# Performance work log

Measured on AMD Instinct MI355X. Metric: run time of the kernel, lower is better.

Reference implementation:

```python
import jax, jax.numpy as jnp
import numpy as np

HIDDEN_DIM = 1024
NUM_HEADS = 8
CONTEXT_LEN = 8
HEAD_DIM = HIDDEN_DIM // NUM_HEADS


def setup_inputs() -> dict:
    key = jax.random.key(0)
    ks = jax.random.split(key, 6)
    B, C, H, W = 32, HIDDEN_DIM, 18, 32
    K = CONTEXT_LEN
    h_current = jax.random.normal(ks[0], (B, C, H, W), dtype=jnp.float32)
    h_buffer = jax.random.normal(ks[1], (K, B, C, H, W), dtype=jnp.float32)
    # Parameters (torch nn.Linear stores weight as [out, in]; y = x @ W.T + b)
    s_qkv = 1.0 / np.sqrt(C)
    W_qkv = jax.random.uniform(ks[2], (3 * C, C), jnp.float32, -s_qkv, s_qkv)
    W_out = jax.random.uniform(ks[3], (C, C), jnp.float32, -s_qkv, s_qkv)
    b_out = jax.random.uniform(ks[4], (C,), jnp.float32, -s_qkv, s_qkv)
    rel_emb = jax.random.normal(ks[5], (2 * CONTEXT_LEN + 1, NUM_HEADS), dtype=jnp.float32)
    return {"h_current": h_current, "h_buffer": h_buffer, "W_qkv": W_qkv,
            "W_out": W_out, "b_out": b_out, "rel_emb": rel_emb}


def reference(h_current, h_buffer, W_qkv, W_out, b_out, rel_emb):
    B, C, H, W = h_current.shape
    K = h_buffer.shape[0]
    T = K + 1
    nh, hd = NUM_HEADS, HEAD_DIM

    # spatial pooling (AdaptiveAvgPool2d(1)) then stack buffer frames + current
    pooled_buf = h_buffer.mean(axis=(3, 4))          # [K, B, C]
    pooled_cur = h_current.mean(axis=(2, 3))         # [B, C]
    context = jnp.concatenate(
        [jnp.transpose(pooled_buf, (1, 0, 2)), pooled_cur[:, None, :]], axis=1)  # [B, T, C]

    # QKV projection (no bias)
    qkv = context @ W_qkv.T                          # [B, T, 3C]
    q, k, v = jnp.split(qkv, 3, axis=-1)
    q = q.reshape(B, T, nh, hd).transpose(0, 2, 1, 3)  # [B, nh, T, hd]
    k = k.reshape(B, T, nh, hd).transpose(0, 2, 1, 3)
    v = v.reshape(B, T, nh, hd).transpose(0, 2, 1, 3)

    # relative-position bias
    idx = jnp.arange(T)
    rel = jnp.clip(idx[:, None] - idx[None, :], -CONTEXT_LEN, CONTEXT_LEN) + CONTEXT_LEN
    bias = rel_emb[rel]                              # [T, T, nh]
    bias = jnp.transpose(bias, (2, 0, 1))            # [nh, T, T]

    # causal mask (-inf above diagonal) combined with bias
    causal = jnp.triu(jnp.full((T, T), -jnp.inf, dtype=context.dtype), k=1)
    attn_mask = causal[None, None, :, :] + bias[None, :, :, :]  # [1, nh, T, T]

    scale = 1.0 / np.sqrt(hd)
    scores = jnp.einsum('bhqd,bhkd->bhqk', q, k) * scale + attn_mask
    attn = jax.nn.softmax(scores, axis=-1)
    attn_out = jnp.einsum('bhqk,bhkd->bhqd', attn, v)  # [B, nh, T, hd]
    attn_out = attn_out.transpose(0, 2, 1, 3).reshape(B, T, C)

    # output projection of final timestep, broadcast over spatial dims, residual
    out = attn_out[:, -1] @ W_out.T + b_out          # [B, C]
    return h_current + out[:, :, None, None]
```

## Files before the change

kernel.cpp:

```cpp
#include <hip/hip_runtime.h>
#include <hip/hip_bf16.h>

#define BB 32
#define CC 1024
#define HWSZ 576
#define KCTX 8
#define TT 9
#define NH 8
#define HD 128

#define GBM 32
#define GBN 128
#define GBK 32

#define NS_KV 8
#define NS_Q  8

#define KV_MN (288 * 2048)
#define Q_MN  (32 * 1024)

typedef float v4f __attribute__((ext_vector_type(4)));

__global__ __launch_bounds__(256) void pool_kernel(
    const float* __restrict__ hbuf,
    const float* __restrict__ hcur,
    float* __restrict__ ctx)
{
    const int wave = threadIdx.x >> 6;
    const int lane = threadIdx.x & 63;
    const int sub  = lane >> 4;
    const int l16  = lane & 15;
    const int stride = gridDim.x * 16;
    const int nrows = BB * TT * CC;

    for (int r0 = (blockIdx.x * 4 + wave) * 4; r0 < nrows; r0 += stride) {
        const int r = r0 + sub;
        v4f acc = {0.f, 0.f, 0.f, 0.f};
        int cidx;
        if (r < KCTX * BB * CC) {
            const v4f* s4 = (const v4f*)(hbuf + (size_t)r * HWSZ);
            const int t = r >> 15;
            const int b = (r >> 10) & 31;
            cidx = (b * TT + t) * CC + (r & (CC - 1));
#pragma unroll
            for (int j = 0; j < 9; ++j)
                acc += __builtin_nontemporal_load(s4 + l16 + 16 * j);
        } else {
            const int rc = r - KCTX * BB * CC;
            const v4f* s4 = (const v4f*)(hcur + (size_t)rc * HWSZ);
            cidx = ((rc >> 10) * TT + KCTX) * CC + (rc & (CC - 1));
#pragma unroll
            for (int j = 0; j < 9; ++j)
                acc += s4[l16 + 16 * j];
        }
        float sum = acc.x + acc.y + acc.z + acc.w;
        sum += __shfl_xor(sum, 1);
        sum += __shfl_xor(sum, 2);
        sum += __shfl_xor(sum, 4);
        sum += __shfl_xor(sum, 8);
        if (l16 == 0) ctx[cidx] = sum * (1.0f / 576.0f);
    }
}

__device__ __forceinline__ void gemm_tile_body(
    const float* __restrict__ Ablk, int lda,
    const float* __restrict__ Bblk, int ldb,
    float* __restrict__ Yout, int ldy,
    int k0, int klen,
    float (*As)[GBK + 4], float (*Bs)[GBN + 4])
{
    const int tid = threadIdx.x;
    const int tx = tid & 15;
    const int ty = tid >> 4;

    float acc0[8], acc1[8];
#pragma unroll
    for (int i = 0; i < 8; ++i) { acc0[i] = 0.f; acc1[i] = 0.f; }

    for (int kt = k0; kt < k0 + klen; kt += GBK) {
        {
            const int row = tid >> 3;
            const int kc = (tid & 7) << 2;
            float4 a = *(const float4*)(Ablk + (size_t)row * lda + kt + kc);
            *(float4*)(&As[row][kc]) = a;
        }
        {
            const int kc = (tid & 7) << 2;
            const int r0 = tid >> 3;
#pragma unroll
            for (int rr = 0; rr < 4; ++rr) {
                const int row = r0 + rr * 32;
                float4 bv = *(const float4*)(Bblk + (size_t)row * ldb + kt + kc);
                Bs[kc + 0][row] = bv.x;
                Bs[kc + 1][row] = bv.y;
                Bs[kc + 2][row] = bv.z;
                Bs[kc + 3][row] = bv.w;
            }
        }
        __syncthreads();

#pragma unroll
        for (int k4 = 0; k4 < GBK; k4 += 4) {
            float4 a0 = *(const float4*)(&As[ty * 2 + 0][k4]);
            float4 a1 = *(const float4*)(&As[ty * 2 + 1][k4]);
            const float a0v[4] = {a0.x, a0.y, a0.z, a0.w};
            const float a1v[4] = {a1.x, a1.y, a1.z, a1.w};
#pragma unroll
            for (int i = 0; i < 4; ++i) {
                float4 blo = *(const float4*)(&Bs[k4 + i][tx * 8]);
                float4 bhi = *(const float4*)(&Bs[k4 + i][tx * 8 + 4]);
                acc0[0] += a0v[i] * blo.x;  acc0[1] += a0v[i] * blo.y;
                acc0[2] += a0v[i] * blo.z;  acc0[3] += a0v[i] * blo.w;
                acc0[4] += a0v[i] * bhi.x;  acc0[5] += a0v[i] * bhi.y;
                acc0[6] += a0v[i] * bhi.z;  acc0[7] += a0v[i] * bhi.w;
                acc1[0] += a1v[i] * blo.x;  acc1[1] += a1v[i] * blo.y;
                acc1[2] += a1v[i] * blo.z;  acc1[3] += a1v[i] * blo.w;
                acc1[4] += a1v[i] * bhi.x;  acc1[5] += a1v[i] * bhi.y;
                acc1[6] += a1v[i] * bhi.z;  acc1[7] += a1v[i] * bhi.w;
            }
        }
        __syncthreads();
    }

    const int col = tx * 8;
    const int row0 = ty * 2;
    float* y0 = Yout + (size_t)row0 * ldy + col;
    float* y1 = y0 + ldy;
    *(float4*)(y0 + 0) = make_float4(acc0[0], acc0[1], acc0[2], acc0[3]);
    *(float4*)(y0 + 4) = make_float4(acc0[4], acc0[5], acc0[6], acc0[7]);
    *(float4*)(y1 + 0) = make_float4(acc1[0], acc1[1], acc1[2], acc1[3]);
    *(float4*)(y1 + 4) = make_float4(acc1[4], acc1[5], acc1[6], acc1[7]);
}

__global__ __launch_bounds__(256) void qkv_gemm(
    const float* __restrict__ ctx, const float* __restrict__ Wqkv,
    float* __restrict__ qpart, float* __restrict__ kvpart)
{
    __shared__ float As[GBM][GBK + 4];
    __shared__ float Bs[GBK][GBN + 4];

    const int bid = blockIdx.x;
    if (bid < NS_Q * 8) {
        const int s = bid & (NS_Q - 1);
        const int bn = bid >> 3;
        gemm_tile_body(ctx + 8 * CC, TT * CC,
                       Wqkv + (size_t)bn * GBN * CC, CC,
                       qpart + (size_t)s * Q_MN + bn * GBN, 1024,
                       s * (1024 / NS_Q), 1024 / NS_Q, As, Bs);
    } else {
        const int rel = bid - NS_Q * 8;
        const int s = rel & (NS_KV - 1);
        const int tile = rel >> 3;
        const int bm = tile >> 4;
        const int bn = tile & 15;
        gemm_tile_body(ctx + (size_t)bm * GBM * CC, CC,
                       Wqkv + (size_t)CC * CC + (size_t)bn * GBN * CC, CC,
                       kvpart + (size_t)s * KV_MN + (size_t)bm * GBM * 2048 + bn * GBN, 2048,
                       s * (1024 / NS_KV), 1024 / NS_KV, As, Bs);
    }
}

__global__ __launch_bounds__(64) void attn_kernel(
    const float* __restrict__ kvpart,
    const float* __restrict__ qpart,
    const float* __restrict__ rel_emb,
    float* __restrict__ attn_out)
{
    const int lane = threadIdx.x;
    const int pair = blockIdx.x;
    const int b = pair >> 3;
    const int h = pair & 7;
    const float scale = 0.08838834764831845f;

    const int qoff = b * CC + h * HD;
    float q1 = 0.f, q2 = 0.f;
#pragma unroll
    for (int s = 0; s < NS_Q; ++s) {
        q1 += qpart[(size_t)s * Q_MN + qoff + lane];
        q2 += qpart[(size_t)s * Q_MN + qoff + lane + 64];
    }
    q1 *= scale; q2 *= scale;

    float sc[TT];
#pragma unroll
    for (int j = 0; j < TT; ++j) {
        const size_t base = (size_t)(b * TT + j) * 2048 + h * HD;
        float k1 = 0.f, k2 = 0.f;
#pragma unroll
        for (int s = 0; s < NS_KV; ++s) {
            k1 += kvpart[(size_t)s * KV_MN + base + lane];
            k2 += kvpart[(size_t)s * KV_MN + base + lane + 64];
        }
        float p = q1 * k1 + q2 * k2;
#pragma unroll
        for (int off = 32; off; off >>= 1) p += __shfl_xor(p, off);
        sc[j] = p + rel_emb[(2 * KCTX - j) * NH + h];
    }
    float m = sc[0];
#pragma unroll
    for (int j = 1; j < TT; ++j) m = fmaxf(m, sc[j]);
    float sum = 0.f;
#pragma unroll
    for (int j = 0; j < TT; ++j) { sc[j] = expf(sc[j] - m); sum += sc[j]; }
    const float inv = 1.0f / sum;

    float a1 = 0.f, a2 = 0.f;
#pragma unroll
    for (int j = 0; j < TT; ++j) {
        const size_t base = (size_t)(b * TT + j) * 2048 + 1024 + h * HD;
        float v1 = 0.f, v2 = 0.f;
#pragma unroll
        for (int s = 0; s < NS_KV; ++s) {
            v1 += kvpart[(size_t)s * KV_MN + base + lane];
            v2 += kvpart[(size_t)s * KV_MN + base + lane + 64];
        }
        a1 += sc[j] * v1;
        a2 += sc[j] * v2;
    }
    attn_out[qoff + lane] = a1 * inv;
    attn_out[qoff + lane + 64] = a2 * inv;
}

__global__ __launch_bounds__(256) void final_fused(
    const float* __restrict__ hc,
    const float* __restrict__ attnb,
    const float* __restrict__ Wout,
    const float* __restrict__ bias,
    float* __restrict__ y)
{
    const int wave = threadIdx.x >> 6;
    const int lane = threadIdx.x & 63;
    const int stride = gridDim.x * 4;
    const int nrows = BB * CC;

    for (int r = blockIdx.x * 4 + wave; r < nrows; r += stride) {
        const int b = r >> 10;
        const int c = r & (CC - 1);

        const v4f* ar = (const v4f*)(attnb + (size_t)b * CC);
        const v4f* wr = (const v4f*)(Wout + (size_t)c * CC);
        v4f acc = {0.f, 0.f, 0.f, 0.f};
#pragma unroll
        for (int j = 0; j < 4; ++j) {
            v4f a = ar[lane + 64 * j];
            v4f w = wr[lane + 64 * j];
            acc += a * w;
        }
        float dot = acc.x + acc.y + acc.z + acc.w;
#pragma unroll
        for (int off = 32; off; off >>= 1) dot += __shfl_xor(dot, off);
        const float add = dot + bias[c];

        const v4f* s4 = (const v4f*)(hc + (size_t)r * HWSZ);
        v4f* d4 = (v4f*)(y + (size_t)r * HWSZ);
        v4f v0 = s4[lane];
        v0.x += add; v0.y += add; v0.z += add; v0.w += add;
        __builtin_nontemporal_store(v0, d4 + lane);
        v4f v1 = s4[lane + 64];
        v1.x += add; v1.y += add; v1.z += add; v1.w += add;
        __builtin_nontemporal_store(v1, d4 + lane + 64);
        if (lane < 16) {
            v4f v2 = s4[lane + 128];
            v2.x += add; v2.y += add; v2.z += add; v2.w += add;
            __builtin_nontemporal_store(v2, d4 + lane + 128);
        }
    }
}

extern "C" void kernel_launch(void* const* d_in, const int* in_sizes, int n_in,
                              void* d_out, int out_size, void* d_ws, size_t ws_size,
                              hipStream_t stream) {
    const float* h_current = (const float*)d_in[0];
    const float* h_buffer  = (const float*)d_in[1];
    const float* W_qkv     = (const float*)d_in[2];
    const float* W_out     = (const float*)d_in[3];
    const float* b_out     = (const float*)d_in[4];
    const float* rel_emb   = (const float*)d_in[5];

    float* ws = (float*)d_ws;
    float* ctx    = ws;
    float* kvpart = ctx + 294912;
    float* qpart  = kvpart + (size_t)NS_KV * KV_MN;
    float* attnb  = qpart + (size_t)NS_Q * Q_MN;

    pool_kernel<<<2048, 256, 0, stream>>>(h_buffer, h_current, ctx);

    qkv_gemm<<<NS_Q * 8 + NS_KV * 144, 256, 0, stream>>>(ctx, W_qkv, qpart, kvpart);

    attn_kernel<<<BB * NH, 64, 0, stream>>>(kvpart, qpart, rel_emb, attnb);

    final_fused<<<2048, 256, 0, stream>>>(h_current, attnb, W_out, b_out, (float*)d_out);
}
```

Before: 165.1 us.

## Replace FP32 QKV GEMM with bf16 MFMA and convert weights in pool kernel

The QKV projection now runs on bf16 MFMA 16x16x32 instructions. Each wave computes a 16x128 tile directly from global memory, with split-K reduced from 8 to 4, which also shrinks the partial buffers the attention kernel has to sum. The pool kernel writes the pooled context as bf16 and converts W_qkv to bf16 on every call. This trades the scalar-FMA GEMM for matrix cores at the cost of an extra weight conversion pass each call and reduced precision.

```diff
diff --git a/kernel.cpp b/kernel.cpp
--- a/kernel.cpp
+++ b/kernel.cpp
@@ -9,22 +9,26 @@
 #define NH 8
 #define HD 128
 
-#define GBM 32
-#define GBN 128
-#define GBK 32
-
-#define NS_KV 8
-#define NS_Q  8
-
+#define NS 4
 #define KV_MN (288 * 2048)
 #define Q_MN  (32 * 1024)
 
 typedef float v4f __attribute__((ext_vector_type(4)));
+typedef __attribute__((ext_vector_type(8))) short  bf16x8;
+typedef __attribute__((ext_vector_type(8))) ushort u16x8;
+typedef __attribute__((ext_vector_type(4))) float  f32x4;
+
+__device__ __forceinline__ ushort f2bf(float f) {
+    uint u = __builtin_bit_cast(uint, f);
+    return (ushort)((u + 0x7FFFu + ((u >> 16) & 1u)) >> 16);
+}
 
 __global__ __launch_bounds__(256) void pool_kernel(
     const float* __restrict__ hbuf,
     const float* __restrict__ hcur,
-    float* __restrict__ ctx)
+    const float* __restrict__ Wqkv,
+    ushort* __restrict__ ctxb,
+    ushort* __restrict__ Wb)
 {
     const int wave = threadIdx.x >> 6;
     const int lane = threadIdx.x & 63;
@@ -58,105 +62,95 @@
         sum += __shfl_xor(sum, 2);
         sum += __shfl_xor(sum, 4);
         sum += __shfl_xor(sum, 8);
-        if (l16 == 0) ctx[cidx] = sum * (1.0f / 576.0f);
-    }
-}
-
-__device__ __forceinline__ void gemm_tile_body(
-    const float* __restrict__ Ablk, int lda,
-    const float* __restrict__ Bblk, int ldb,
-    float* __restrict__ Yout, int ldy,
-    int k0, int klen,
-    float (*As)[GBK + 4], float (*Bs)[GBN + 4])
-{
-    const int tid = threadIdx.x;
-    const int tx = tid & 15;
-    const int ty = tid >> 4;
-
-    float acc0[8], acc1[8];
-#pragma unroll
-    for (int i = 0; i < 8; ++i) { acc0[i] = 0.f; acc1[i] = 0.f; }
-
-    for (int kt = k0; kt < k0 + klen; kt += GBK) {
-        {
-            const int row = tid >> 3;
-            const int kc = (tid & 7) << 2;
-            float4 a = *(const float4*)(Ablk + (size_t)row * lda + kt + kc);
-            *(float4*)(&As[row][kc]) = a;
-        }
-        {
-            const int kc = (tid & 7) << 2;
-            const int r0 = tid >> 3;
-#pragma unroll
-            for (int rr = 0; rr < 4; ++rr) {
-                const int row = r0 + rr * 32;
-                float4 bv = *(const float4*)(Bblk + (size_t)row * ldb + kt + kc);
-                Bs[kc + 0][row] = bv.x;
-                Bs[kc + 1][row] = bv.y;
-                Bs[kc + 2][row] = bv.z;
-                Bs[kc + 3][row] = bv.w;
-            }
-        }
-        __syncthreads();
-
-#pragma unroll
-        for (int k4 = 0; k4 < GBK; k4 += 4) {
-            float4 a0 = *(const float4*)(&As[ty * 2 + 0][k4]);
-            float4 a1 = *(const float4*)(&As[ty * 2 + 1][k4]);
-            const float a0v[4] = {a0.x, a0.y, a0.z, a0.w};
-            const float a1v[4] = {a1.x, a1.y, a1.z, a1.w};
-#pragma unroll
-            for (int i = 0; i < 4; ++i) {
-                float4 blo = *(const float4*)(&Bs[k4 + i][tx * 8]);
-                float4 bhi = *(const float4*)(&Bs[k4 + i][tx * 8 + 4]);
-                acc0[0] += a0v[i] * blo.x;  acc0[1] += a0v[i] * blo.y;
-                acc0[2] += a0v[i] * blo.z;  acc0[3] += a0v[i] * blo.w;
-                acc0[4] += a0v[i] * bhi.x;  acc0[5] += a0v[i] * bhi.y;
-                acc0[6] += a0v[i] * bhi.z;  acc0[7] += a0v[i] * bhi.w;
-                acc1[0] += a1v[i] * blo.x;  acc1[1] += a1v[i] * blo.y;
-                acc1[2] += a1v[i] * blo.z;  acc1[3] += a1v[i] * blo.w;
-                acc1[4] += a1v[i] * bhi.x;  acc1[5] += a1v[i] * bhi.y;
-                acc1[6] += a1v[i] * bhi.z;  acc1[7] += a1v[i] * bhi.w;
-            }
-        }
-        __syncthreads();
-    }
-
-    const int col = tx * 8;
-    const int row0 = ty * 2;
-    float* y0 = Yout + (size_t)row0 * ldy + col;
-    float* y1 = y0 + ldy;
-    *(float4*)(y0 + 0) = make_float4(acc0[0], acc0[1], acc0[2], acc0[3]);
-    *(float4*)(y0 + 4) = make_float4(acc0[4], acc0[5], acc0[6], acc0[7]);
-    *(float4*)(y1 + 0) = make_float4(acc1[0], acc1[1], acc1[2], acc1[3]);
-    *(float4*)(y1 + 4) = make_float4(acc1[4], acc1[5], acc1[6], acc1[7]);
-}
-
-__global__ __launch_bounds__(256) void qkv_gemm(
-    const float* __restrict__ ctx, const float* __restrict__ Wqkv,
+        if (l16 == 0) ctxb[cidx] = f2bf(sum * (1.0f / 576.0f));
+    }
+
+    const int nchunk = 3072 * 1024 / 8;
+    for (int idx = blockIdx.x * 256 + threadIdx.x; idx < nchunk;
+         idx += gridDim.x * 256) {
+        const float* src = Wqkv + (size_t)idx * 8;
+        v4f a = *(const v4f*)src;
+        v4f b = *(const v4f*)(src + 4);
+        u16x8 o;
+        o[0] = f2bf(a.x); o[1] = f2bf(a.y); o[2] = f2bf(a.z); o[3] = f2bf(a.w);
+        o[4] = f2bf(b.x); o[5] = f2bf(b.y); o[6] = f2bf(b.z); o[7] = f2bf(b.w);
+        *(u16x8*)(Wb + (size_t)idx * 8) = o;
+    }
+}
+
+__global__ __launch_bounds__(256) void qkv_mfma(
+    const ushort* __restrict__ ctxb, const ushort* __restrict__ Wb,
     float* __restrict__ qpart, float* __restrict__ kvpart)
 {
-    __shared__ float As[GBM][GBK + 4];
-    __shared__ float Bs[GBK][GBN + 4];
-
-    const int bid = blockIdx.x;
-    if (bid < NS_Q * 8) {
-        const int s = bid & (NS_Q - 1);
-        const int bn = bid >> 3;
-        gemm_tile_body(ctx + 8 * CC, TT * CC,
-                       Wqkv + (size_t)bn * GBN * CC, CC,
-                       qpart + (size_t)s * Q_MN + bn * GBN, 1024,
-                       s * (1024 / NS_Q), 1024 / NS_Q, As, Bs);
+    const int wave = threadIdx.x >> 6;
+    const int lane = threadIdx.x & 63;
+    const int t = blockIdx.x * 4 + wave;
+    const int l15 = lane & 15;
+    const int kg  = lane >> 4;
+
+    const ushort* abase;
+    const ushort* bbase;
+    float* out;
+    int ldy, outrow0, outcol0;
+
+    if (t < 1152) {
+        const int s  = t & 3;
+        const int tt = t >> 2;
+        const int mt = tt / 16, nt = tt % 16;
+        const int k0 = s * 256;
+        abase = ctxb + (size_t)(mt * 16 + l15) * 1024 + k0 + kg * 8;
+        bbase = Wb + (size_t)(1024 + nt * 128 + l15) * 1024 + k0 + kg * 8;
+        out = kvpart + (size_t)s * KV_MN;
+        ldy = 2048;
+        outrow0 = mt * 16 + kg * 4;
+        outcol0 = nt * 128 + l15;
     } else {
-        const int rel = bid - NS_Q * 8;
-        const int s = rel & (NS_KV - 1);
-        const int tile = rel >> 3;
-        const int bm = tile >> 4;
-        const int bn = tile & 15;
-        gemm_tile_body(ctx + (size_t)bm * GBM * CC, CC,
-                       Wqkv + (size_t)CC * CC + (size_t)bn * GBN * CC, CC,
-                       kvpart + (size_t)s * KV_MN + (size_t)bm * GBM * 2048 + bn * GBN, 2048,
-                       s * (1024 / NS_KV), 1024 / NS_KV, As, Bs);
+        const int r  = t - 1152;
+        const int s  = r & 3;
+        const int tt = r >> 2;
+        const int mt = tt >> 3, nt = tt & 7;
+        const int k0 = s * 256;
+        abase = ctxb + (size_t)((mt * 16 + l15) * 9 + 8) * 1024 + k0 + kg * 8;
+        bbase = Wb + (size_t)(nt * 128 + l15) * 1024 + k0 + kg * 8;
+        out = qpart + (size_t)s * Q_MN;
+        ldy = 1024;
+        outrow0 = mt * 16 + kg * 4;
+        outcol0 = nt * 128 + l15;
+    }
+
+    f32x4 acc0 = {0,0,0,0}, acc1 = {0,0,0,0}, acc2 = {0,0,0,0}, acc3 = {0,0,0,0};
+    f32x4 acc4 = {0,0,0,0}, acc5 = {0,0,0,0}, acc6 = {0,0,0,0}, acc7 = {0,0,0,0};
+
+#pragma unroll
+    for (int kk = 0; kk < 8; ++kk) {
+        bf16x8 a = *(const bf16x8*)(abase + kk * 32);
+        const ushort* bp = bbase + kk * 32;
+        bf16x8 b0 = *(const bf16x8*)(bp + 0 * 16 * 1024);
+        bf16x8 b1 = *(const bf16x8*)(bp + 1 * 16 * 1024);
+        bf16x8 b2 = *(const bf16x8*)(bp + 2 * 16 * 1024);
+        bf16x8 b3 = *(const bf16x8*)(bp + 3 * 16 * 1024);
+        bf16x8 b4 = *(const bf16x8*)(bp + 4 * 16 * 1024);
+        bf16x8 b5 = *(const bf16x8*)(bp + 5 * 16 * 1024);
+        bf16x8 b6 = *(const bf16x8*)(bp + 6 * 16 * 1024);
+        bf16x8 b7 = *(const bf16x8*)(bp + 7 * 16 * 1024);
+        acc0 = __builtin_amdgcn_mfma_f32_16x16x32_bf16(a, b0, acc0, 0, 0, 0);
+        acc1 = __builtin_amdgcn_mfma_f32_16x16x32_bf16(a, b1, acc1, 0, 0, 0);
+        acc2 = __builtin_amdgcn_mfma_f32_16x16x32_bf16(a, b2, acc2, 0, 0, 0);
+        acc3 = __builtin_amdgcn_mfma_f32_16x16x32_bf16(a, b3, acc3, 0, 0, 0);
+        acc4 = __builtin_amdgcn_mfma_f32_16x16x32_bf16(a, b4, acc4, 0, 0, 0);
+        acc5 = __builtin_amdgcn_mfma_f32_16x16x32_bf16(a, b5, acc5, 0, 0, 0);
+        acc6 = __builtin_amdgcn_mfma_f32_16x16x32_bf16(a, b6, acc6, 0, 0, 0);
+        acc7 = __builtin_amdgcn_mfma_f32_16x16x32_bf16(a, b7, acc7, 0, 0, 0);
+    }
+
+    float* yb = out + (size_t)outrow0 * ldy + outcol0;
+#pragma unroll
+    for (int i = 0; i < 4; ++i) {
+        float* yr = yb + (size_t)i * ldy;
+        yr[0 * 16] = acc0[i]; yr[1 * 16] = acc1[i];
+        yr[2 * 16] = acc2[i]; yr[3 * 16] = acc3[i];
+        yr[4 * 16] = acc4[i]; yr[5 * 16] = acc5[i];
+        yr[6 * 16] = acc6[i]; yr[7 * 16] = acc7[i];
     }
 }
 
@@ -175,7 +169,7 @@
     const int qoff = b * CC + h * HD;
     float q1 = 0.f, q2 = 0.f;
 #pragma unroll
-    for (int s = 0; s < NS_Q; ++s) {
+    for (int s = 0; s < NS; ++s) {
         q1 += qpart[(size_t)s * Q_MN + qoff + lane];
         q2 += qpart[(size_t)s * Q_MN + qoff + lane + 64];
     }
@@ -187,7 +181,7 @@
         const size_t base = (size_t)(b * TT + j) * 2048 + h * HD;
         float k1 = 0.f, k2 = 0.f;
 #pragma unroll
-        for (int s = 0; s < NS_KV; ++s) {
+        for (int s = 0; s < NS; ++s) {
             k1 += kvpart[(size_t)s * KV_MN + base + lane];
             k2 += kvpart[(size_t)s * KV_MN + base + lane + 64];
         }
@@ -210,7 +204,7 @@
         const size_t base = (size_t)(b * TT + j) * 2048 + 1024 + h * HD;
         float v1 = 0.f, v2 = 0.f;
 #pragma unroll
-        for (int s = 0; s < NS_KV; ++s) {
+        for (int s = 0; s < NS; ++s) {
             v1 += kvpart[(size_t)s * KV_MN + base + lane];
             v2 += kvpart[(size_t)s * KV_MN + base + lane + 64];
         }
@@ -277,15 +271,15 @@
     const float* b_out     = (const float*)d_in[4];
     const float* rel_emb   = (const float*)d_in[5];
 
-    float* ws = (float*)d_ws;
-    float* ctx    = ws;
-    float* kvpart = ctx + 294912;
-    float* qpart  = kvpart + (size_t)NS_KV * KV_MN;
-    float* attnb  = qpart + (size_t)NS_Q * Q_MN;
-
-    pool_kernel<<<2048, 256, 0, stream>>>(h_buffer, h_current, ctx);
-
-    qkv_gemm<<<NS_Q * 8 + NS_KV * 144, 256, 0, stream>>>(ctx, W_qkv, qpart, kvpart);
+    ushort* ctxb = (ushort*)d_ws;
+    ushort* Wb   = ctxb + 294912;
+    float* kvpart = (float*)(Wb + 3145728);
+    float* qpart  = kvpart + (size_t)NS * KV_MN;
+    float* attnb  = qpart + (size_t)NS * Q_MN;
+
+    pool_kernel<<<2048, 256, 0, stream>>>(h_buffer, h_current, W_qkv, ctxb, Wb);
+
+    qkv_mfma<<<304, 256, 0, stream>>>(ctxb, Wb, qpart, kvpart);
 
     attn_kernel<<<BB * NH, 64, 0, stream>>>(kvpart, qpart, rel_emb, attnb);
 
```

New measurement: 154.6 us, median of 2. 6.4% less time.
